# Kernel optimization log

Hardware: AMD Instinct MI355X
Metric: run time of the kernel (lower is better)

Reference implementation:

```python
import jax, jax.numpy as jnp
import numpy as np

CHUNK, OVERLAP = 4096, 1024
STRIDE = CHUNK - OVERLAP            # 3072
NFFT, HOP = 1024, 256
F = NFFT // 2 + 1                   # 513
NF = (CHUNK - NFFT) // HOP + 1      # 13 frames per chunk (center=False)
H, E = 256, 128
B, C, T = 8, 1, 480000


def setup_inputs() -> dict:
    key = jax.random.key(0)
    ks = jax.random.split(key, 8)
    s = lambda d: 1.0 / np.sqrt(d)
    return {
        "audio": jax.random.normal(ks[0], (B, C, T), jnp.float32),
        "emb_table": jax.random.normal(ks[1], (16, E), jnp.float32) * 0.1,
        "gru_wx": jax.random.normal(ks[2], (F + E, 3 * H), jnp.float32) * s(F + E),
        "gru_wh": jax.random.normal(ks[3], (H, 3 * H), jnp.float32) * s(H),
        "gru_b": jnp.zeros((3 * H,), jnp.float32),
        "proj_w": jax.random.normal(ks[4], (H, 2 * F), jnp.float32) * s(H),
        "proj_b": jnp.zeros((2 * F,), jnp.float32),
        "effect_id": jax.random.randint(ks[5], (B,), 0, 16),
    }


def _hann(n):
    return (0.5 - 0.5 * jnp.cos(2.0 * jnp.pi * jnp.arange(n) / n)).astype(jnp.float32)


def _film(mag, emb, gru_wx, gru_wh, gru_b, proj_w, proj_b):
    # mag: [B, C, K, NF, F]; emb: [B, E]
    b, c, k, nf, f = mag.shape
    emb_b = jnp.broadcast_to(emb[:, None, None, None, :], (b, c, k, nf, E))
    x = jnp.concatenate([mag, emb_b], axis=-1).reshape(b * c * k, nf, f + E)
    xg = x @ gru_wx                                   # [M, NF, 3H]
    h0 = jnp.zeros((b * c * k, H), mag.dtype)

    def step(h, xg_t):
        hg = h @ gru_wh + gru_b
        z = jax.nn.sigmoid(xg_t[:, :H] + hg[:, :H])
        r = jax.nn.sigmoid(xg_t[:, H:2 * H] + hg[:, H:2 * H])
        n = jnp.tanh(xg_t[:, 2 * H:] + r * hg[:, 2 * H:])
        h = (1.0 - z) * n + z * h
        return h, h

    _, hs = jax.lax.scan(step, h0, jnp.swapaxes(xg, 0, 1))  # [NF, M, H]
    hs = jnp.swapaxes(hs, 0, 1)                              # [M, NF, H]
    gb = hs @ proj_w + proj_b                                # [M, NF, 2F]
    gamma, beta = gb[..., :F], gb[..., F:]
    gamma = gamma.reshape(b, c, k, nf, f)
    beta = beta.reshape(b, c, k, nf, f)
    return gamma * mag + beta


def reference(audio, emb_table, gru_wx, gru_wh, gru_b, proj_w, proj_b, effect_id):
    win = _hann(NFFT)
    emb = emb_table[effect_id]                              # [B, E]

    t = audio.shape[-1]
    n_chunks = -(-t // STRIDE)                              # 157
    t_pad = (n_chunks - 1) * STRIDE + CHUNK
    xp = jnp.pad(audio, ((0, 0), (0, 0), (0, t_pad - t)))

    cidx = jnp.arange(n_chunks)[:, None] * STRIDE + jnp.arange(CHUNK)  # [K, CHUNK]
    chunks = xp[..., cidx]                                  # [B, C, K, CHUNK]

    fidx = jnp.arange(NF)[:, None] * HOP + jnp.arange(NFFT)  # [NF, NFFT]
    frames = chunks[..., fidx] * win                         # [B, C, K, NF, NFFT]
    spec = jnp.fft.rfft(frames, axis=-1)                     # [B, C, K, NF, F]

    mag = jnp.abs(spec)
    phase = jnp.angle(spec)
    mod_mag = _film(mag, emb, gru_wx, gru_wh, gru_b, proj_w, proj_b)
    comp = jax.lax.complex(mod_mag * jnp.cos(phase), mod_mag * jnp.sin(phase))

    y = jnp.fft.irfft(comp, n=NFFT, axis=-1) * win           # [B, C, K, NF, NFFT]
    rec = jnp.zeros_like(chunks).at[..., fidx].add(y)        # OLA within chunk
    wsum = jnp.zeros((CHUNK,), jnp.float32).at[fidx].add(win ** 2)
    rec = rec / jnp.maximum(wsum, 1e-8)

    out = jnp.zeros_like(xp).at[..., cidx].add(rec)          # OLA across chunks
    return out[..., :t]
```

## Files before the change

### kernel.cpp

```cpp
#include <hip/hip_runtime.h>
#include <math.h>

#define T_LEN    480000
#define NB       8
#define NK       157
#define CHUNKSZ  4096
#define STRIDESZ 3072
#define NFFT_SZ  1024
#define HOP_SZ   256
#define NFREQ    513
#define NFR      13
#define HDIM     256
#define EDIM     128
#define GDIM     768
#define PDIM     1026
#define FR_STRIDE 1026
#define NFRAMES  (NB*NK*NFR)
#define NCHUNKS  (NB*NK)
#define KCF      2041

#define XG_KS    17
#define XG_NB    3
#define PJ_KS    8
#define PJ_NB    5
#define GRU_CT   5

#define TWO_PI_D 6.283185307179586

typedef short bf16x8 __attribute__((ext_vector_type(8)));
typedef float f32x4  __attribute__((ext_vector_type(4)));

__device__ __forceinline__ void split_bf16(float v, short& hi, short& lo) {
  unsigned u = __float_as_uint(v);
  hi = (short)(u >> 16);
  float fh = __uint_as_float(u & 0xFFFF0000u);
  float res = v - fh;
  lo = (short)(__float_as_uint(res) >> 16);
}

__device__ __forceinline__ unsigned short f2bf(float v) {
  unsigned u = __float_as_uint(v);
  u += 0x7FFFu + ((u >> 16) & 1u);
  return (unsigned short)(u >> 16);
}
__device__ __forceinline__ float bf2f(unsigned short b) {
  return __uint_as_float(((unsigned)b) << 16);
}

__device__ __forceinline__ void fft512x2(float (*re)[512], float (*im)[512],
                                         const float* twc, const float* tws,
                                         int tid, float dir) {
  int q = tid >> 7;
  int j = tid & 127;
  #pragma unroll
  for (int s = 1; s <= 7; s += 2) {
    int half = 1 << (s - 1);
    int p   = j & (half - 1);
    int grp = j >> (s - 1);
    int i0  = grp * 4 * half + p;
    int i1  = i0 + half;
    int i2  = i0 + 2 * half;
    int i3  = i0 + 3 * half;
    float r0 = re[q][i0], q0 = im[q][i0], r1 = re[q][i1], q1 = im[q][i1];
    float r2 = re[q][i2], q2 = im[q][i2], r3 = re[q][i3], q3 = im[q][i3];
    int qa = p << (10 - s);
    float ca = twc[qa], sa = dir * tws[qa];
    float tr = ca * r1 - sa * q1, ti = ca * q1 + sa * r1;
    float u0r = r0 + tr, u0i = q0 + ti;
    float u1r = r0 - tr, u1i = q0 - ti;
    tr = ca * r3 - sa * q3; ti = ca * q3 + sa * r3;
    float u2r = r2 + tr, u2i = q2 + ti;
    float u3r = r2 - tr, u3i = q2 - ti;
    int qb = p << (9 - s);
    int qc = (p + half) << (9 - s);
    float cb = twc[qb], sb = dir * tws[qb];
    float cc = twc[qc], sc = dir * tws[qc];
    tr = cb * u2r - sb * u2i; ti = cb * u2i + sb * u2r;
    re[q][i0] = u0r + tr; im[q][i0] = u0i + ti;
    re[q][i2] = u0r - tr; im[q][i2] = u0i - ti;
    tr = cc * u3r - sc * u3i; ti = cc * u3i + sc * u3r;
    re[q][i1] = u1r + tr; im[q][i1] = u1i + ti;
    re[q][i3] = u1r - tr; im[q][i3] = u1i - ti;
    __syncthreads();
  }
  {
    int p = tid;
    int qd = p << 1;
    float c = twc[qd], sn = dir * tws[qd];
    #pragma unroll
    for (int f = 0; f < 2; ++f) {
      int i1 = p, i2 = p + 256;
      float r2 = re[f][i2], q2 = im[f][i2];
      float tr = c * r2 - sn * q2;
      float ti = c * q2 + sn * r2;
      float r1 = re[f][i1], q1 = im[f][i1];
      re[f][i2] = r1 - tr; im[f][i2] = q1 - ti;
      re[f][i1] = r1 + tr; im[f][i1] = q1 + ti;
    }
    __syncthreads();
  }
}

__global__ void k_tables(float* __restrict__ win, float* __restrict__ wsinv,
                         float* __restrict__ twc, float* __restrict__ tws) {
  int tid = threadIdx.x;
  for (int i = tid; i < NFFT_SZ; i += 256) {
    double w = 0.5 - 0.5 * cos((TWO_PI_D / (double)NFFT_SZ) * (double)i);
    win[i] = (float)w;
  }
  for (int i = tid; i < 512; i += 256) {
    double th = (TWO_PI_D / (double)NFFT_SZ) * (double)i;
    twc[i] = (float)cos(th);
    tws[i] = (float)sin(th);
  }
  for (int pc = tid; pc < CHUNKSZ; pc += 256) {
    int t1 = min(NFR - 1, pc >> 8);
    int t0 = (pc > NFFT_SZ - 1) ? ((pc - 768) >> 8) : 0;
    float ws = 0.f;
    for (int tt = t0; tt <= t1; ++tt) {
      int n = pc - tt * HOP_SZ;
      double w = 0.5 - 0.5 * cos((TWO_PI_D / (double)NFFT_SZ) * (double)n);
      float wf = (float)w;
      ws += wf * wf;
    }
    wsinv[pc] = 1.0f / fmaxf(ws, 1e-8f);
  }
}

__global__ void k_prep(const float* __restrict__ wx,
                       short* __restrict__ wxb_hi, short* __restrict__ wxb_lo) {
  int id = blockIdx.x * 256 + threadIdx.x;
  if (id >= XG_NB * XG_KS * 256) return;
  int nb  = id / (XG_KS * 256);
  int ks  = (id / 256) % XG_KS;
  int col = id % 256;
  int col_g = nb * 256 + col;
  size_t base = (size_t)id * 32;
  for (int j = 0; j < 32; ++j) {
    int k_g = ks * 32 + j;
    float v = wx[(size_t)k_g * GDIM + col_g];
    short hi, lo;
    split_bf16(v, hi, lo);
    wxb_hi[base + j] = hi;
    wxb_lo[base + j] = lo;
  }
}

__global__ void k_prep_wht(const float* __restrict__ wh, float4* __restrict__ whT4) {
  int id = blockIdx.x * 256 + threadIdx.x;
  if (id >= 64 * GDIM) return;
  int k4  = id / GDIM;
  int col = id % GDIM;
  whT4[id] = make_float4(wh[(size_t)(k4 * 4 + 0) * GDIM + col],
                         wh[(size_t)(k4 * 4 + 1) * GDIM + col],
                         wh[(size_t)(k4 * 4 + 2) * GDIM + col],
                         wh[(size_t)(k4 * 4 + 3) * GDIM + col]);
}

__global__ void k_prep_pw(const float* __restrict__ pw,
                          short* __restrict__ pwb_hi, short* __restrict__ pwb_lo) {
  int id = blockIdx.x * 256 + threadIdx.x;
  if (id >= PJ_NB * PJ_KS * 256) return;
  int nb  = id / (PJ_KS * 256);
  int ks  = (id / 256) % PJ_KS;
  int col = id % 256;
  int col_g = nb * 256 + col;
  size_t base = (size_t)id * 32;
  for (int j = 0; j < 32; ++j) {
    int k_g = ks * 32 + j;
    float v = (col_g < PDIM) ? pw[(size_t)k_g * PDIM + col_g] : 0.f;
    short hi, lo;
    split_bf16(v, hi, lo);
    pwb_hi[base + j] = hi;
    pwb_lo[base + j] = lo;
  }
}

__global__ void k_embxg(const float* __restrict__ emb_table, const int* __restrict__ effect_id,
                        const float* __restrict__ wx, float* __restrict__ embxg) {
  int b = blockIdx.x;
  int tid = threadIdx.x;
  int e_id = effect_id[b];
  const float* ev = emb_table + (size_t)e_id * EDIM;
  #pragma unroll
  for (int j = 0; j < 3; ++j) {
    int col = tid + 256 * j;
    float acc = 0.f;
    #pragma unroll 4
    for (int e = 0; e < EDIM; ++e)
      acc += ev[e] * wx[(size_t)(NFREQ + e) * GDIM + col];
    embxg[(size_t)b * GDIM + col] = acc;
  }
}

__global__ void k_stft(const float* __restrict__ audio, const float* __restrict__ win,
                       const float* __restrict__ gtwc, const float* __restrict__ gtws,
                       unsigned* __restrict__ spec) {
  int fr0 = blockIdx.x * 2;
  int tid = threadIdx.x;
  __shared__ float xin[2][NFFT_SZ];
  __shared__ float re[2][512], im[2][512];
  __shared__ float twc[512], tws[512];
  for (int i = tid; i < 512; i += 256) { twc[i] = gtwc[i]; tws[i] = gtws[i]; }
  for (int i = tid; i < 2 * NFFT_SZ; i += 256) {
    int q = i >> 10, ii = i & 1023;
    int fr = fr0 + q;
    int b   = fr / KCF;
    int rem = fr % KCF;
    int k = rem / NFR, t = rem % NFR;
    int pos = k * STRIDESZ + t * HOP_SZ + ii;
    float v = (pos < T_LEN) ? audio[b * T_LEN + pos] : 0.f;
    xin[q][ii] = v * win[ii];
  }
  __syncthreads();
  for (int i = tid; i < 1024; i += 256) {
    int q = i >> 9, n = i & 511;
    int rv = (int)(__brev((unsigned)n) >> 23);
    re[q][n] = xin[q][2 * rv];
    im[q][n] = xin[q][2 * rv + 1];
  }
  __syncthreads();
  fft512x2(re, im, twc, tws, tid, -1.f);
  for (int i = tid; i < 1024; i += 256) {
    int q = i >> 9, k = i & 511;
    int m = (512 - k) & 511;
    float zr = re[q][k],  zi = im[q][k];
    float mr = re[q][m],  mi = -im[q][m];
    float xer = 0.5f * (zr + mr), xei = 0.5f * (zi + mi);
    float dr  = 0.5f * (zr - mr), di  = 0.5f * (zi - mi);
    float xor_ = di, xoi = -dr;
    float c = twc[k], s = tws[k];
    float Xr = xer + c * xor_ + s * xoi;
    float Xi = xei + c * xoi - s * xor_;
    unsigned* sp = spec + (size_t)(fr0 + q) * (FR_STRIDE / 2);
    sp[k] = (((unsigned)f2bf(Xi)) << 16) | (unsigned)f2bf(Xr);
  }
  if (tid < 2) {
    int q = tid;
    float Xr = re[q][0] - im[q][0];
    unsigned* sp = spec + (size_t)(fr0 + q) * (FR_STRIDE / 2);
    sp[512] = (((unsigned)f2bf(0.f)) << 16) | (unsigned)f2bf(Xr);
  }
}

__global__ __launch_bounds__(256) void k_xg(
    const unsigned* __restrict__ spec, const float* __restrict__ embxg,
    const short* __restrict__ wxb_hi, const short* __restrict__ wxb_lo,
    float* __restrict__ xg) {
  int nb  = blockIdx.x % XG_NB;
  int mb  = blockIdx.x / XG_NB;
  int fr0 = mb * 64;
  int tid = threadIdx.x;
  int lane = tid & 63;
  int wv   = tid >> 6;

  __shared__ __align__(16) short lsA[2][64 * 40];
  __shared__ __align__(16) short lsB[2][256 * 40];

  f32x4 acc[4][4];
  #pragma unroll
  for (int i = 0; i < 4; ++i)
    #pragma unroll
    for (int j = 0; j < 4; ++j)
      acc[i][j] = (f32x4){0.f, 0.f, 0.f, 0.f};

  int lrow = lane & 15;
  int lk8  = (lane >> 4) * 8;

  for (int ks = 0; ks < XG_KS; ++ks) {
    int k0 = ks * 32;
    {
      int f = tid >> 2, q = tid & 3;
      int fr = fr0 + f;
      short hi[8], lo[8];
      #pragma unroll
      for (int j = 0; j < 8; ++j) {
        int bg = k0 + q * 8 + j;
        float m = 0.f;
        if (fr < NFRAMES && bg <= 512) {
          unsigned pv = spec[(size_t)fr * (FR_STRIDE / 2) + bg];
          float rr = bf2f((unsigned short)(pv & 0xFFFFu));
          float ii = bf2f((unsigned short)(pv >> 16));
          m = sqrtf(rr * rr + ii * ii);
        }
        split_bf16(m, hi[j], lo[j]);
      }
      int off = f * 40 + q * 8;
      *(bf16x8*)&lsA[0][off] = *(bf16x8*)hi;
      *(bf16x8*)&lsA[1][off] = *(bf16x8*)lo;
    }
    {
      const short* gh = wxb_hi + (((size_t)nb * XG_KS + ks) * 256 + tid) * 32;
      const short* gl = wxb_lo + (((size_t)nb * XG_KS + ks) * 256 + tid) * 32;
      int off = tid * 40;
      #pragma unroll
      for (int i = 0; i < 4; ++i) {
        *(bf16x8*)&lsB[0][off + 8 * i] = *(const bf16x8*)(gh + 8 * i);
        *(bf16x8*)&lsB[1][off + 8 * i] = *(const bf16x8*)(gl + 8 * i);
      }
    }
    __syncthreads();
    bf16x8 aH[4], aL[4], bH[4], bL[4];
    #pragma unroll
    for (int mt = 0; mt < 4; ++mt) {
      int off = (16 * mt + lrow) * 40 + lk8;
      aH[mt] = *(const bf16x8*)&lsA[0][off];
      aL[mt] = *(const bf16x8*)&lsA[1][off];
    }
    #pragma unroll
    for (int nt = 0; nt < 4; ++nt) {
      int col = wv * 64 + nt * 16 + lrow;
      int off = col * 40 + lk8;
      bH[nt] = *(const bf16x8*)&lsB[0][off];
      bL[nt] = *(const bf16x8*)&lsB[1][off];
    }
    #pragma unroll
    for (int mt = 0; mt < 4; ++mt)
      #pragma unroll
      for (int nt = 0; nt < 4; ++nt) {
        acc[mt][nt] = __builtin_amdgcn_mfma_f32_16x16x32_bf16(aH[mt], bH[nt], acc[mt][nt], 0, 0, 0);
        acc[mt][nt] = __builtin_amdgcn_mfma_f32_16x16x32_bf16(aH[mt], bL[nt], acc[mt][nt], 0, 0, 0);
        acc[mt][nt] = __builtin_amdgcn_mfma_f32_16x16x32_bf16(aL[mt], bH[nt], acc[mt][nt], 0, 0, 0);
      }
    __syncthreads();
  }

  int ncol0 = nb * 256 + wv * 64;
  #pragma unroll
  for (int mt = 0; mt < 4; ++mt) {
    #pragma unroll
    for (int r = 0; r < 4; ++r) {
      int fr = fr0 + mt * 16 + (lane >> 4) * 4 + r;
      if (fr < NFRAMES) {
        int b = fr / KCF;
        #pragma unroll
        for (int nt = 0; nt < 4; ++nt) {
          int col = ncol0 + nt * 16 + (lane & 15);
          xg[(size_t)fr * GDIM + col] = acc[mt][nt][r] + embxg[(size_t)b * GDIM + col];
        }
      }
    }
  }
}

__global__ __launch_bounds__(768) void k_gru(
    const float* __restrict__ xg, const float4* __restrict__ whT4,
    const float* __restrict__ bias, float* __restrict__ hs) {
  int c0 = blockIdx.x * GRU_CT;
  int tid = threadIdx.x;
  __shared__ __align__(16) float h[GRU_CT][HDIM];
  __shared__ float hg[GRU_CT][GDIM];
  float* hflat = &h[0][0];
  for (int i = tid; i < GRU_CT * HDIM; i += 768) hflat[i] = 0.f;
  float bcol = bias[tid];
  __syncthreads();
  for (int t = 0; t < NFR; ++t) {
    float acc[GRU_CT];
    #pragma unroll
    for (int c = 0; c < GRU_CT; ++c) acc[c] = bcol;
    const float4* wp = whT4 + tid;
    #pragma unroll 2
    for (int k = 0; k < HDIM; k += 4) {
      float4 w = *wp;
      wp += GDIM;
      #pragma unroll
      for (int c = 0; c < GRU_CT; ++c) {
        float4 hv = *(const float4*)&h[c][k];
        acc[c] += hv.x * w.x + hv.y * w.y + hv.z * w.z + hv.w * w.w;
      }
    }
    #pragma unroll
    for (int c = 0; c < GRU_CT; ++c) hg[c][tid] = acc[c];
    __syncthreads();
    for (int i = tid; i < GRU_CT * HDIM; i += 768) {
      int c = i >> 8, u = i & 255;
      int cb = c0 + c;
      if (cb < NCHUNKS) {
        const float* xgt = xg + (size_t)(cb * NFR + t) * GDIM;
        float z = 1.f / (1.f + expf(-(xgt[u] + hg[c][u])));
        float r = 1.f / (1.f + expf(-(xgt[u + 256] + hg[c][u + 256])));
        float n = tanhf(xgt[u + 512] + r * hg[c][u + 512]);
        float hn = (1.f - z) * n + z * h[c][u];
        h[c][u] = hn;
        hs[(size_t)(cb * NFR + t) * HDIM + u] = hn;
      }
    }
    __syncthreads();
  }
}

__global__ __launch_bounds__(256) void k_proj(
    const float* __restrict__ hs, const short* __restrict__ pwb_hi,
    const short* __restrict__ pwb_lo, const float* __restrict__ pb,
    unsigned short* __restrict__ gb) {
  int nb  = blockIdx.x % PJ_NB;
  int mb  = blockIdx.x / PJ_NB;
  int fr0 = mb * 64;
  int tid = threadIdx.x;
  int lane = tid & 63;
  int wv   = tid >> 6;

  __shared__ __align__(16) short lsA[2][64 * 40];
  __shared__ __align__(16) short lsB[2][256 * 40];

  f32x4 acc[4][4];
  #pragma unroll
  for (int i = 0; i < 4; ++i)
    #pragma unroll
    for (int j = 0; j < 4; ++j)
      acc[i][j] = (f32x4){0.f, 0.f, 0.f, 0.f};

  int lrow = lane & 15;
  int lk8  = (lane >> 4) * 8;

  for (int ks = 0; ks < PJ_KS; ++ks) {
    {
      int f = tid >> 2, q = tid & 3;
      int fr = fr0 + f;
      float v[8];
      if (fr < NFRAMES) {
        const float* src = hs + (size_t)fr * HDIM + ks * 32 + q * 8;
        float4 v0 = *(const float4*)src;
        float4 v1 = *(const float4*)(src + 4);
        v[0]=v0.x; v[1]=v0.y; v[2]=v0.z; v[3]=v0.w;
        v[4]=v1.x; v[5]=v1.y; v[6]=v1.z; v[7]=v1.w;
      } else {
        #pragma unroll
        for (int j = 0; j < 8; ++j) v[j] = 0.f;
      }
      short hi[8], lo[8];
      #pragma unroll
      for (int j = 0; j < 8; ++j) split_bf16(v[j], hi[j], lo[j]);
      int off = f * 40 + q * 8;
      *(bf16x8*)&lsA[0][off] = *(bf16x8*)hi;
      *(bf16x8*)&lsA[1][off] = *(bf16x8*)lo;
    }
    {
      const short* gh = pwb_hi + (((size_t)nb * PJ_KS + ks) * 256 + tid) * 32;
      const short* gl = pwb_lo + (((size_t)nb * PJ_KS + ks) * 256 + tid) * 32;
      int off = tid * 40;
      #pragma unroll
      for (int i = 0; i < 4; ++i) {
        *(bf16x8*)&lsB[0][off + 8 * i] = *(const bf16x8*)(gh + 8 * i);
        *(bf16x8*)&lsB[1][off + 8 * i] = *(const bf16x8*)(gl + 8 * i);
      }
    }
    __syncthreads();
    bf16x8 aH[4], aL[4], bH[4], bL[4];
    #pragma unroll
    for (int mt = 0; mt < 4; ++mt) {
      int off = (16 * mt + lrow) * 40 + lk8;
      aH[mt] = *(const bf16x8*)&lsA[0][off];
      aL[mt] = *(const bf16x8*)&lsA[1][off];
    }
    #pragma unroll
    for (int nt = 0; nt < 4; ++nt) {
      int col = wv * 64 + nt * 16 + lrow;
      int off = col * 40 + lk8;
      bH[nt] = *(const bf16x8*)&lsB[0][off];
      bL[nt] = *(const bf16x8*)&lsB[1][off];
    }
    #pragma unroll
    for (int mt = 0; mt < 4; ++mt)
      #pragma unroll
      for (int nt = 0; nt < 4; ++nt) {
        acc[mt][nt] = __builtin_amdgcn_mfma_f32_16x16x32_bf16(aH[mt], bH[nt], acc[mt][nt], 0, 0, 0);
        acc[mt][nt] = __builtin_amdgcn_mfma_f32_16x16x32_bf16(aH[mt], bL[nt], acc[mt][nt], 0, 0, 0);
        acc[mt][nt] = __builtin_amdgcn_mfma_f32_16x16x32_bf16(aL[mt], bH[nt], acc[mt][nt], 0, 0, 0);
      }
    __syncthreads();
  }

  int ncol0 = nb * 256 + wv * 64;
  float pbv[4];
  int cols[4];
  #pragma unroll
  for (int nt = 0; nt < 4; ++nt) {
    cols[nt] = ncol0 + nt * 16 + (lane & 15);
    pbv[nt] = (cols[nt] < PDIM) ? pb[cols[nt]] : 0.f;
  }
  #pragma unroll
  for (int mt = 0; mt < 4; ++mt) {
    #pragma unroll
    for (int r = 0; r < 4; ++r) {
      int fr = fr0 + mt * 16 + (lane >> 4) * 4 + r;
      if (fr < NFRAMES) {
        #pragma unroll
        for (int nt = 0; nt < 4; ++nt) {
          if (cols[nt] < PDIM)
            gb[(size_t)fr * PDIM + cols[nt]] = f2bf(acc[mt][nt][r] + pbv[nt]);
        }
      }
    }
  }
}

__global__ void k_istft(unsigned* __restrict__ spec, const unsigned short* __restrict__ gb,
                        const float* __restrict__ win, const float* __restrict__ wsinv,
                        const float* __restrict__ gtwc, const float* __restrict__ gtws) {
  int fr0 = blockIdx.x * 2;
  int tid = threadIdx.x;
  __shared__ float sre[2][NFREQ], sim[2][NFREQ];
  __shared__ float re[2][512], im[2][512];
  __shared__ float twc[512], tws[512];
  for (int i = tid; i < 512; i += 256) { twc[i] = gtwc[i]; tws[i] = gtws[i]; }
  for (int i = tid; i < 2 * NFREQ; i += 256) {
    int q = (i >= NFREQ) ? 1 : 0;
    int f = i - q * NFREQ;
    int fr = fr0 + q;
    unsigned pv = spec[(size_t)fr * (FR_STRIDE / 2) + f];
    float r  = bf2f((unsigned short)(pv & 0xFFFFu));
    float iv = bf2f((unsigned short)(pv >> 16));
    float mag = sqrtf(r * r + iv * iv);
    const unsigned short* gbrow = gb + (size_t)fr * PDIM;
    float gamma = bf2f(gbrow[f]);
    float beta  = bf2f(gbrow[NFREQ + f]);
    float mm = gamma * mag + beta;
    float nr, ni;
    if (mag > 0.f) {
      float s = mm / mag;
      nr = r * s; ni = iv * s;
    } else {
      nr = mm; ni = 0.f;
    }
    sre[q][f] = nr;
    sim[q][f] = (f == 0 || f == NFREQ - 1) ? 0.f : ni;
  }
  __syncthreads();
  for (int i = tid; i < 1024; i += 256) {
    int q = i >> 9, n = i & 511;
    int k = (int)(__brev((unsigned)n) >> 23);
    float Xr = sre[q][k],       Xi = sim[q][k];
    float Mr = sre[q][512 - k], Mi = -sim[q][512 - k];
    float xer = 0.5f * (Xr + Mr), xei = 0.5f * (Xi + Mi);
    float dr  = 0.5f * (Xr - Mr), di  = 0.5f * (Xi - Mi);
    float c = twc[k], s = tws[k];
    float xor_ = c * dr - s * di;
    float xoi  = c * di + s * dr;
    re[q][n] = xer - xoi;
    im[q][n] = xei + xor_;
  }
  __syncthreads();
  fft512x2(re, im, twc, tws, tid, +1.f);
  for (int i = tid; i < 1024; i += 256) {
    int q = i >> 9, n = i & 511;
    int fr = fr0 + q;
    int t = fr % NFR;
    int ia = 2 * n, ib = 2 * n + 1;
    float ya = re[q][n] * (1.0f / 512.0f) * win[ia] * wsinv[t * HOP_SZ + ia];
    float yb = im[q][n] * (1.0f / 512.0f) * win[ib] * wsinv[t * HOP_SZ + ib];
    unsigned* sp = spec + (size_t)fr * (FR_STRIDE / 2);
    sp[n] = (((unsigned)f2bf(yb)) << 16) | (unsigned)f2bf(ya);
  }
}

__global__ void k_gather(const unsigned short* __restrict__ ybuf, float* __restrict__ out) {
  int gid = blockIdx.x * 256 + threadIdx.x;
  if (gid >= NB * T_LEN) return;
  int b = gid / T_LEN, pos = gid % T_LEN;
  float acc = 0.f;
  int k_hi = min(NK - 1, pos / STRIDESZ);
  int k_lo = (pos >= CHUNKSZ) ? ((pos - (CHUNKSZ - 1) + (STRIDESZ - 1)) / STRIDESZ) : 0;
  for (int k = k_lo; k <= k_hi; ++k) {
    int pc = pos - k * STRIDESZ;
    int t1 = min(NFR - 1, pc >> 8);
    int t0 = (pc > NFFT_SZ - 1) ? ((pc - 768) >> 8) : 0;
    int frbase = (b * NK + k) * NFR;
    for (int tt = t0; tt <= t1; ++tt) {
      acc += bf2f(ybuf[(size_t)(frbase + tt) * FR_STRIDE + (pc - tt * HOP_SZ)]);
    }
  }
  out[gid] = acc;
}

extern "C" void kernel_launch(void* const* d_in, const int* in_sizes, int n_in,
                              void* d_out, int out_size, void* d_ws, size_t ws_size,
                              hipStream_t stream) {
  const float* audio     = (const float*)d_in[0];
  const float* emb_table = (const float*)d_in[1];
  const float* gru_wx    = (const float*)d_in[2];
  const float* gru_wh    = (const float*)d_in[3];
  const float* gru_b     = (const float*)d_in[4];
  const float* proj_w    = (const float*)d_in[5];
  const float* proj_b    = (const float*)d_in[6];
  const int*   effect_id = (const int*)d_in[7];
  float* out = (float*)d_out;

  char* base = (char*)d_ws;
  size_t off = 0;
  auto alloc = [&](size_t bytes) { char* p = base + off; off = (off + bytes + 255) & ~(size_t)255; return p; };
  unsigned* spec   = (unsigned*)alloc((size_t)NFRAMES * FR_STRIDE * 2);
  float*    xg     = (float*)   alloc((size_t)NFRAMES * GDIM * 4);
  float*    hs     = (float*)   alloc((size_t)NFRAMES * HDIM * 4);
  float*    win    = (float*)   alloc(NFFT_SZ * 4);
  float*    wsinv  = (float*)   alloc(CHUNKSZ * 4);
  float*    twc    = (float*)   alloc(512 * 4);
  float*    tws    = (float*)   alloc(512 * 4);
  float*    embxg  = (float*)   alloc(NB * GDIM * 4);
  short*    wxb_hi = (short*)   alloc((size_t)XG_NB * XG_KS * 256 * 32 * 2);
  short*    wxb_lo = (short*)   alloc((size_t)XG_NB * XG_KS * 256 * 32 * 2);
  short*    pwb_hi = (short*)   alloc((size_t)PJ_NB * PJ_KS * 256 * 32 * 2);
  short*    pwb_lo = (short*)   alloc((size_t)PJ_NB * PJ_KS * 256 * 32 * 2);
  float4*   whT4   = (float4*)  alloc((size_t)64 * GDIM * 16);
  unsigned short* gb = (unsigned short*)xg;

  k_tables  <<<1, 256, 0, stream>>>(win, wsinv, twc, tws);
  k_embxg   <<<NB, 256, 0, stream>>>(emb_table, effect_id, gru_wx, embxg);
  k_prep    <<<(XG_NB * XG_KS * 256 + 255) / 256, 256, 0, stream>>>(gru_wx, wxb_hi, wxb_lo);
  k_prep_wht<<<(64 * GDIM + 255) / 256, 256, 0, stream>>>(gru_wh, whT4);
  k_prep_pw <<<(PJ_NB * PJ_KS * 256 + 255) / 256, 256, 0, stream>>>(proj_w, pwb_hi, pwb_lo);
  k_stft    <<<NFRAMES / 2, 256, 0, stream>>>(audio, win, twc, tws, spec);
  k_xg      <<<256 * XG_NB, 256, 0, stream>>>(spec, embxg, wxb_hi, wxb_lo, xg);
  k_gru     <<<(NCHUNKS + GRU_CT - 1) / GRU_CT, 768, 0, stream>>>(xg, whT4, gru_b, hs);
  k_proj    <<<256 * PJ_NB, 256, 0, stream>>>(hs, pwb_hi, pwb_lo, proj_b, gb);
  k_istft   <<<NFRAMES / 2, 256, 0, stream>>>(spec, gb, win, wsinv, twc, tws);
  k_gather  <<<(NB * T_LEN + 255) / 256, 256, 0, stream>>>((const unsigned short*)spec, out);
}
```

Measured before the change: 541.5 us.

## Compute all three GRU gates per thread and drop shared hg buffer

The GRU recurrence kernel now uses 256 threads per block. Each thread computes the z, r and n gate columns for one hidden unit in registers, instead of 768 threads each writing one gate column to shared memory. This removes the shared hg buffer, one barrier-separated pass per step, and the shared-memory round trip for gate values. The trade-off is three times the registers and work per thread and fewer waves per block, which could lower latency hiding in this serial recurrence.

```diff
diff --git a/kernel.cpp b/kernel.cpp
--- a/kernel.cpp
+++ b/kernel.cpp
@@ -343,46 +343,47 @@
   }
 }
 
-__global__ __launch_bounds__(768) void k_gru(
+__global__ __launch_bounds__(256) void k_gru(
     const float* __restrict__ xg, const float4* __restrict__ whT4,
     const float* __restrict__ bias, float* __restrict__ hs) {
   int c0 = blockIdx.x * GRU_CT;
   int tid = threadIdx.x;
   __shared__ __align__(16) float h[GRU_CT][HDIM];
-  __shared__ float hg[GRU_CT][GDIM];
-  float* hflat = &h[0][0];
-  for (int i = tid; i < GRU_CT * HDIM; i += 768) hflat[i] = 0.f;
-  float bcol = bias[tid];
+  for (int i = tid; i < GRU_CT * HDIM; i += 256) (&h[0][0])[i] = 0.f;
+  float b0 = bias[tid], b1 = bias[tid + 256], b2 = bias[tid + 512];
   __syncthreads();
   for (int t = 0; t < NFR; ++t) {
-    float acc[GRU_CT];
-    #pragma unroll
-    for (int c = 0; c < GRU_CT; ++c) acc[c] = bcol;
+    float a0[GRU_CT], a1[GRU_CT], a2[GRU_CT];
+    #pragma unroll
+    for (int c = 0; c < GRU_CT; ++c) { a0[c] = b0; a1[c] = b1; a2[c] = b2; }
     const float4* wp = whT4 + tid;
     #pragma unroll 2
     for (int k = 0; k < HDIM; k += 4) {
-      float4 w = *wp;
+      float4 w0 = wp[0];
+      float4 w1 = wp[256];
+      float4 w2 = wp[512];
       wp += GDIM;
       #pragma unroll
       for (int c = 0; c < GRU_CT; ++c) {
         float4 hv = *(const float4*)&h[c][k];
-        acc[c] += hv.x * w.x + hv.y * w.y + hv.z * w.z + hv.w * w.w;
-      }
-    }
-    #pragma unroll
-    for (int c = 0; c < GRU_CT; ++c) hg[c][tid] = acc[c];
-    __syncthreads();
-    for (int i = tid; i < GRU_CT * HDIM; i += 768) {
-      int c = i >> 8, u = i & 255;
+        a0[c] = fmaf(hv.x, w0.x, a0[c]); a1[c] = fmaf(hv.x, w1.x, a1[c]); a2[c] = fmaf(hv.x, w2.x, a2[c]);
+        a0[c] = fmaf(hv.y, w0.y, a0[c]); a1[c] = fmaf(hv.y, w1.y, a1[c]); a2[c] = fmaf(hv.y, w2.y, a2[c]);
+        a0[c] = fmaf(hv.z, w0.z, a0[c]); a1[c] = fmaf(hv.z, w1.z, a1[c]); a2[c] = fmaf(hv.z, w2.z, a2[c]);
+        a0[c] = fmaf(hv.w, w0.w, a0[c]); a1[c] = fmaf(hv.w, w1.w, a1[c]); a2[c] = fmaf(hv.w, w2.w, a2[c]);
+      }
+    }
+    __syncthreads();
+    #pragma unroll
+    for (int c = 0; c < GRU_CT; ++c) {
       int cb = c0 + c;
       if (cb < NCHUNKS) {
         const float* xgt = xg + (size_t)(cb * NFR + t) * GDIM;
-        float z = 1.f / (1.f + expf(-(xgt[u] + hg[c][u])));
-        float r = 1.f / (1.f + expf(-(xgt[u + 256] + hg[c][u + 256])));
-        float n = tanhf(xgt[u + 512] + r * hg[c][u + 512]);
-        float hn = (1.f - z) * n + z * h[c][u];
-        h[c][u] = hn;
-        hs[(size_t)(cb * NFR + t) * HDIM + u] = hn;
+        float z = 1.f / (1.f + expf(-(xgt[tid] + a0[c])));
+        float r = 1.f / (1.f + expf(-(xgt[tid + 256] + a1[c])));
+        float n = tanhf(xgt[tid + 512] + r * a2[c]);
+        float hn = (1.f - z) * n + z * h[c][tid];
+        h[c][tid] = hn;
+        hs[(size_t)(cb * NFR + t) * HDIM + tid] = hn;
       }
     }
     __syncthreads();
@@ -611,7 +612,7 @@
   k_prep_pw <<<(PJ_NB * PJ_KS * 256 + 255) / 256, 256, 0, stream>>>(proj_w, pwb_hi, pwb_lo);
   k_stft    <<<NFRAMES / 2, 256, 0, stream>>>(audio, win, twc, tws, spec);
   k_xg      <<<256 * XG_NB, 256, 0, stream>>>(spec, embxg, wxb_hi, wxb_lo, xg);
-  k_gru     <<<(NCHUNKS + GRU_CT - 1) / GRU_CT, 768, 0, stream>>>(xg, whT4, gru_b, hs);
+  k_gru     <<<(NCHUNKS + GRU_CT - 1) / GRU_CT, 256, 0, stream>>>(xg, whT4, gru_b, hs);
   k_proj    <<<256 * PJ_NB, 256, 0, stream>>>(hs, pwb_hi, pwb_lo, proj_b, gb);
   k_istft   <<<NFRAMES / 2, 256, 0, stream>>>(spec, gb, win, wsinv, twc, tws);
   k_gather  <<<(NB * T_LEN + 255) / 256, 256, 0, stream>>>((const unsigned short*)spec, out);
```

New measurement: 541.3 us. About the same (-0.0%).
